# Performance work log

Hardware: AMD Instinct MI355X
Metric: run time of the kernel (lower is better)

Reference implementation:

```python
import jax, jax.numpy as jnp
import numpy as np

B, C, H, W = 16, 192, 48, 48
D_STATE, DT_RANK, D_INNER, K = 16, 16, 288, 4


def setup_inputs() -> dict:
    key = jax.random.key(0)
    ks = jax.random.split(key, 8)
    g = lambda k, shape, scale: jax.random.normal(k, shape, jnp.float32) * scale
    # S4D-real style init: A_log = log(1..N)
    A_log = jnp.tile(jnp.log(jnp.arange(1.0, D_STATE + 1.0, dtype=jnp.float32)), (K, D_INNER, 1))
    return {
        "x": jax.random.normal(ks[0], (B, C, H, W), jnp.float32),
        "W_in": g(ks[1], (C, 2 * D_INNER), C ** -0.5),
        "conv_w": g(ks[2], (D_INNER, 1, 3, 3), 1.0 / 3.0),
        "conv_b": jnp.zeros((D_INNER,), jnp.float32),
        "x_proj_w": g(ks[3], (K, DT_RANK + 2 * D_STATE, D_INNER), D_INNER ** -0.5),
        "dt_w": g(ks[4], (K, D_INNER, DT_RANK), DT_RANK ** -0.5),
        "dt_b": g(ks[5], (K, D_INNER), 0.5) - 4.0,
        "A_log": A_log,
        "Ds": jnp.ones((K, D_INNER), jnp.float32),
        "ln_g": jnp.ones((D_INNER,), jnp.float32),
        "ln_b": jnp.zeros((D_INNER,), jnp.float32),
        "W_out": g(ks[6], (D_INNER, C), D_INNER ** -0.5),
        "bn_g": jnp.ones((C,), jnp.float32),
        "bn_b": jnp.zeros((C,), jnp.float32),
    }


def reference(x, W_in, conv_w, conv_b, x_proj_w, dt_w, dt_b, A_log, Ds,
              ln_g, ln_b, W_out, bn_g, bn_b):
    b, c, h, w = x.shape
    L = h * w
    # MambaBlock: NCHW -> NHWC, SS2D(v2), NHWC -> NCHW, BatchNorm2d
    xhwc = jnp.transpose(x, (0, 2, 3, 1))                        # (B,H,W,C)
    xz = xhwc @ W_in                                             # (B,H,W,2*Di)
    xc, z = jnp.split(xz, 2, axis=-1)
    # depthwise 3x3 conv + SiLU
    xc = jnp.transpose(xc, (0, 3, 1, 2))                         # (B,Di,H,W)
    xc = jax.lax.conv_general_dilated(
        xc, conv_w, (1, 1), ((1, 1), (1, 1)),
        dimension_numbers=('NCHW', 'OIHW', 'NCHW'),
        feature_group_count=D_INNER)
    xc = jax.nn.silu(xc + conv_b[None, :, None, None])
    # cross-scan: 4 directions (row-major, col-major, + reversals)
    x_hw = xc.reshape(b, D_INNER, L)
    x_wh = jnp.transpose(xc, (0, 1, 3, 2)).reshape(b, D_INNER, L)
    xs = jnp.stack([x_hw, x_wh], axis=1)
    xs = jnp.concatenate([xs, jnp.flip(xs, axis=-1)], axis=1)    # (B,K,Di,L)
    # input-dependent dt, B, C
    x_dbl = jnp.einsum('bkdl,kcd->bkcl', xs, x_proj_w)
    dts, Bmat, Cmat = jnp.split(x_dbl, [DT_RANK, DT_RANK + D_STATE], axis=2)
    dt = jnp.einsum('bkrl,kdr->bkdl', dts, dt_w)
    dt = jax.nn.softplus(dt + dt_b[None, :, :, None])            # (B,K,Di,L)
    A = -jnp.exp(A_log)                                          # (K,Di,N)
    # selective scan along L (sequential recurrence)
    us = jnp.transpose(xs, (3, 0, 1, 2))                         # (L,B,K,Di)
    dts_t = jnp.transpose(dt, (3, 0, 1, 2))
    Bs_t = jnp.transpose(Bmat, (3, 0, 1, 2))                     # (L,B,K,N)
    Cs_t = jnp.transpose(Cmat, (3, 0, 1, 2))

    def step(hst, inp):
        u_t, d_t, B_t, C_t = inp
        dA = jnp.exp(d_t[..., None] * A)                         # (B,K,Di,N)
        hst = dA * hst + (d_t * u_t)[..., None] * B_t[:, :, None, :]
        y_t = jnp.sum(hst * C_t[:, :, None, :], axis=-1)         # (B,K,Di)
        return hst, y_t

    h0 = jnp.zeros((b, K, D_INNER, D_STATE), xs.dtype)
    _, ys = jax.lax.scan(step, h0, (us, dts_t, Bs_t, Cs_t))
    ys = jnp.transpose(ys, (1, 2, 3, 0))                         # (B,K,Di,L)
    ys = ys + Ds[None, :, :, None] * xs                          # skip (D) term
    # cross-merge: undo flips / transpose and sum the 4 directions
    y = ys[:, 0] + jnp.flip(ys[:, 2], axis=-1)
    y_wh = ys[:, 1] + jnp.flip(ys[:, 3], axis=-1)                # col-major order
    y = y + jnp.transpose(y_wh.reshape(b, D_INNER, w, h), (0, 1, 3, 2)).reshape(b, D_INNER, L)
    y = jnp.transpose(y.reshape(b, D_INNER, h, w), (0, 2, 3, 1))  # (B,H,W,Di)
    # out_norm (LayerNorm over channels), gating, out projection
    mu = jnp.mean(y, axis=-1, keepdims=True)
    var = jnp.var(y, axis=-1, keepdims=True)
    y = (y - mu) * jax.lax.rsqrt(var + 1e-5) * ln_g + ln_b
    y = y * jax.nn.silu(z)
    out = jnp.transpose(y @ W_out, (0, 3, 1, 2))                 # (B,C,H,W)
    # BatchNorm2d (training-mode batch statistics)
    m = jnp.mean(out, axis=(0, 2, 3), keepdims=True)
    v = jnp.var(out, axis=(0, 2, 3), keepdims=True)
    out = (out - m) * jax.lax.rsqrt(v + 1e-5) * bn_g[None, :, None, None] + bn_b[None, :, None, None]
    return out
```

## Files before the change

### kernel.cpp

```cpp
#include <hip/hip_runtime.h>
#include <hip/hip_fp16.h>
#include <math.h>

#define BB 16
#define CC 192
#define LL 2304
#define DI 288
#define NS 16

__device__ __forceinline__ float softplus_f(float v) {
  return v > 15.f ? v : __logf(1.f + __expf(v));
}

__device__ __forceinline__ int pos_of(int k, int t) {
  int tt = (k >= 2) ? (2303 - t) : t;
  if (k & 1) return (tt % 48) * 48 + tt / 48;
  return tt;
}
__device__ __forceinline__ int invpos(int k, int l) {
  int tt = (k & 1) ? (l % 48) * 48 + l / 48 : l;
  return (k >= 2) ? (2303 - tt) : tt;
}

__device__ __forceinline__ void pow_table(float E, float* P) {
  float p2 = E * E, p4 = p2 * p2, p8 = p4 * p4;
  P[0] = E;       P[1] = p2;      P[2] = p2 * E;  P[3] = p4;
  P[4] = p4 * E;  P[5] = p4 * p2; P[6] = p4 * P[2]; P[7] = p8;
  P[8] = p8 * E;  P[9] = p8 * p2; P[10] = p8 * P[2]; P[11] = p8 * p4;
  P[12] = p8 * P[4]; P[13] = p8 * P[5]; P[14] = p8 * P[6]; P[15] = p8 * p8;
}

__global__ __launch_bounds__(256) void k_wT(const float* __restrict__ xpw,
                                            float* __restrict__ wT) {
  int i = blockIdx.x * 256 + threadIdx.x;
  if (i >= DI * CC) return;
  int d = i % DI, j = i / DI;
  wT[d * CC + j] = xpw[j * DI + d];
}

__global__ __launch_bounds__(256) void k_check(const float* __restrict__ alog,
                                               int* __restrict__ flag) {
  __shared__ int ok;
  if (threadIdx.x == 0) ok = 1;
  __syncthreads();
  int bad = 0;
  for (int i = threadIdx.x; i < 4 * DI * NS; i += 256) {
    int n = i & 15;
    float t = __logf((float)(n + 1));
    if (fabsf(alog[i] - t) > 1e-5f) bad = 1;
  }
  if (bad) atomicAnd(&ok, 0);
  __syncthreads();
  if (threadIdx.x == 0) *flag = ok;
}

__global__ __launch_bounds__(256) void g_inproj(const float* __restrict__ x,
                                                const float* __restrict__ Win,
                                                float* __restrict__ xc,
                                                float* __restrict__ z) {
  __shared__ float Asm[48 * 128];
  __shared__ float Bsm[48 * 64];
  int nt = blockIdx.x % 9, mt = blockIdx.x / 9;
  int b = mt / 18, l0 = (mt % 18) * 128;
  int j0 = nt * 64;
  int tl = threadIdx.x & 15, tj = threadIdx.x >> 4;
  float acc[8][4];
#pragma unroll
  for (int i = 0; i < 8; ++i)
#pragma unroll
    for (int m = 0; m < 4; ++m) acc[i][m] = 0.f;
  for (int kt = 0; kt < 4; ++kt) {
    int k0 = kt * 48;
    __syncthreads();
    for (int i = threadIdx.x; i < 1536; i += 256) {
      int c = i >> 5, lq = i & 31;
      *(float4*)&Asm[c * 128 + lq * 4] =
          *(const float4*)&x[((size_t)b * CC + k0 + c) * LL + l0 + lq * 4];
    }
    for (int i = threadIdx.x; i < 768; i += 256) {
      int c = i >> 4, jq = i & 15;
      *(float4*)&Bsm[c * 64 + jq * 4] =
          *(const float4*)&Win[(size_t)(k0 + c) * 576 + j0 + jq * 4];
    }
    __syncthreads();
    for (int k = 0; k < 48; ++k) {
      float4 a0 = *(float4*)&Asm[k * 128 + tl * 8];
      float4 a1 = *(float4*)&Asm[k * 128 + tl * 8 + 4];
      float4 bv = *(float4*)&Bsm[k * 64 + tj * 4];
      float av[8] = {a0.x, a0.y, a0.z, a0.w, a1.x, a1.y, a1.z, a1.w};
      float bw[4] = {bv.x, bv.y, bv.z, bv.w};
#pragma unroll
      for (int i = 0; i < 8; ++i)
#pragma unroll
        for (int m = 0; m < 4; ++m) acc[i][m] = fmaf(av[i], bw[m], acc[i][m]);
    }
  }
  int jbase = j0 + tj * 4;
  if (jbase < DI) {
#pragma unroll
    for (int i = 0; i < 8; ++i) {
      int l = l0 + tl * 8 + i;
      *(float4*)&xc[((size_t)b * LL + l) * DI + jbase] =
          make_float4(acc[i][0], acc[i][1], acc[i][2], acc[i][3]);
    }
  } else {
    int j2 = jbase - DI;
#pragma unroll
    for (int m = 0; m < 4; ++m) {
      *(float4*)&z[((size_t)b * DI + j2 + m) * LL + l0 + tl * 8] =
          make_float4(acc[0][m], acc[1][m], acc[2][m], acc[3][m]);
      *(float4*)&z[((size_t)b * DI + j2 + m) * LL + l0 + tl * 8 + 4] =
          make_float4(acc[4][m], acc[5][m], acc[6][m], acc[7][m]);
    }
  }
}

__global__ __launch_bounds__(288) void k_conv2(const float* __restrict__ xc,
                                               const float* __restrict__ cw,
                                               const float* __restrict__ cb,
                                               float* __restrict__ co) {
  int b = blockIdx.x / 48, h = blockIdx.x % 48;
  int d = threadIdx.x;
  float wv[9];
#pragma unroll
  for (int j = 0; j < 9; ++j) wv[j] = cw[d * 9 + j];
  float bias = cb[d];
  bool hm = h > 0, hp = h < 47;
  const float* row0 = xc + ((size_t)b * LL + (h - 1) * 48) * DI + d;
  const float* row1 = xc + ((size_t)b * LL + h * 48) * DI + d;
  const float* row2 = xc + ((size_t)b * LL + (h + 1) * 48) * DI + d;
  float* op = co + ((size_t)b * LL + h * 48) * DI + d;
  float a0 = 0.f, a1 = 0.f, a2 = 0.f;
  float b0, b1, b2, c0, c1, c2;
  b0 = hm ? row0[0] : 0.f;
  b1 = row1[0];
  b2 = hp ? row2[0] : 0.f;
  for (int w = 0; w < 48; ++w) {
    if (w < 47) {
      int off = (w + 1) * DI;
      c0 = hm ? row0[off] : 0.f;
      c1 = row1[off];
      c2 = hp ? row2[off] : 0.f;
    } else {
      c0 = 0.f; c1 = 0.f; c2 = 0.f;
    }
    float acc = bias;
    acc = fmaf(a0, wv[0], acc); acc = fmaf(b0, wv[1], acc); acc = fmaf(c0, wv[2], acc);
    acc = fmaf(a1, wv[3], acc); acc = fmaf(b1, wv[4], acc); acc = fmaf(c1, wv[5], acc);
    acc = fmaf(a2, wv[6], acc); acc = fmaf(b2, wv[7], acc); acc = fmaf(c2, wv[8], acc);
    acc = acc / (1.f + __expf(-acc));
    op[w * DI] = acc;
    a0 = b0; a1 = b1; a2 = b2;
    b0 = c0; b1 = c1; b2 = c2;
  }
}

__global__ __launch_bounds__(256) void g_xdbl(const float* __restrict__ co,
                                              const float* __restrict__ wT,
                                              float* __restrict__ xd) {
  __shared__ float Asm[48 * 132];
  __shared__ float Bsm[48 * 64];
  int nt = blockIdx.x % 3, mt = blockIdx.x / 3;
  int b = mt / 18, l0 = (mt % 18) * 128;
  int j0 = nt * 64;
  int tl = threadIdx.x & 15, tj = threadIdx.x >> 4;
  float acc[8][4];
#pragma unroll
  for (int i = 0; i < 8; ++i)
#pragma unroll
    for (int m = 0; m < 4; ++m) acc[i][m] = 0.f;
  for (int kt = 0; kt < 6; ++kt) {
    int k0 = kt * 48;
    __syncthreads();
    for (int i = threadIdx.x; i < 1536; i += 256) {
      int l = i / 12, dq = i % 12;
      float4 v = *(const float4*)&co[((size_t)b * LL + l0 + l) * DI + k0 + dq * 4];
      Asm[(dq * 4 + 0) * 132 + l] = v.x;
      Asm[(dq * 4 + 1) * 132 + l] = v.y;
      Asm[(dq * 4 + 2) * 132 + l] = v.z;
      Asm[(dq * 4 + 3) * 132 + l] = v.w;
    }
    for (int i = threadIdx.x; i < 768; i += 256) {
      int c = i >> 4, jq = i & 15;
      *(float4*)&Bsm[c * 64 + jq * 4] =
          *(const float4*)&wT[(size_t)(k0 + c) * CC + j0 + jq * 4];
    }
    __syncthreads();
    for (int k = 0; k < 48; ++k) {
      float4 a0 = *(float4*)&Asm[k * 132 + tl * 8];
      float4 a1 = *(float4*)&Asm[k * 132 + tl * 8 + 4];
      float4 bv = *(float4*)&Bsm[k * 64 + tj * 4];
      float av[8] = {a0.x, a0.y, a0.z, a0.w, a1.x, a1.y, a1.z, a1.w};
      float bw[4] = {bv.x, bv.y, bv.z, bv.w};
#pragma unroll
      for (int i = 0; i < 8; ++i)
#pragma unroll
        for (int m = 0; m < 4; ++m) acc[i][m] = fmaf(av[i], bw[m], acc[i][m]);
    }
  }
  int j = j0 + tj * 4;
  int kk = j / 48, c2 = j % 48;
#pragma unroll
  for (int i = 0; i < 8; ++i) {
    int l = l0 + tl * 8 + i;
    *(float4*)&xd[(((size_t)b * 4 + kk) * LL + l) * 48 + c2] =
        make_float4(acc[i][0], acc[i][1], acc[i][2], acc[i][3]);
  }
}

__global__ __launch_bounds__(288) void g_dt(const float* __restrict__ xd,
                                            const float* __restrict__ dtw,
                                            const float* __restrict__ dtb,
                                            __half* __restrict__ dth) {
  int blk = blockIdx.x;
  int lc = blk % 72, bk = blk / 72;
  int k = bk & 3;
  int d = threadIdx.x;
  float w_dt[16];
#pragma unroll
  for (int r4 = 0; r4 < 4; ++r4) {
    float4 t4 = *(const float4*)&dtw[((size_t)k * DI + d) * 16 + r4 * 4];
    w_dt[r4 * 4 + 0] = t4.x; w_dt[r4 * 4 + 1] = t4.y;
    w_dt[r4 * 4 + 2] = t4.z; w_dt[r4 * 4 + 3] = t4.w;
  }
  float bias = dtb[k * DI + d];
  const float* __restrict__ xb = xd + (size_t)bk * LL * 48;
  __half* __restrict__ Eb = dth + (size_t)bk * LL * DI;
#pragma unroll 2
  for (int j = 0; j < 32; ++j) {
    int l = lc * 32 + j;
    const float* __restrict__ xr = xb + (size_t)l * 48;
    float4 v0 = *(const float4*)(xr + 0);
    float4 v1 = *(const float4*)(xr + 4);
    float4 v2 = *(const float4*)(xr + 8);
    float4 v3 = *(const float4*)(xr + 12);
    float a0 = fmaf(v0.x, w_dt[0], bias);
    float a1 = v0.y * w_dt[1];
    float a2 = v0.z * w_dt[2];
    float a3 = v0.w * w_dt[3];
    a0 = fmaf(v1.x, w_dt[4], a0); a1 = fmaf(v1.y, w_dt[5], a1);
    a2 = fmaf(v1.z, w_dt[6], a2); a3 = fmaf(v1.w, w_dt[7], a3);
    a0 = fmaf(v2.x, w_dt[8], a0); a1 = fmaf(v2.y, w_dt[9], a1);
    a2 = fmaf(v2.z, w_dt[10], a2); a3 = fmaf(v2.w, w_dt[11], a3);
    a0 = fmaf(v3.x, w_dt[12], a0); a1 = fmaf(v3.y, w_dt[13], a1);
    a2 = fmaf(v3.z, w_dt[14], a2); a3 = fmaf(v3.w, w_dt[15], a3);
    float v = (a0 + a1) + (a2 + a3);
    float dt = v > 15.f ? v : __logf(1.f + __expf(v));
    int t = invpos(k, l);
    Eb[(size_t)t * DI + d] = __float2half(dt);
  }
}

template <int SCHT, bool USE_E>
__global__ __launch_bounds__(288) void k_pass1(const float* __restrict__ co,
                                               const float* __restrict__ xd,
                                               const float* __restrict__ dtw,
                                               const float* __restrict__ dtb,
                                               const float* __restrict__ alog,
                                               const int* __restrict__ flag,
                                               const __half* __restrict__ dth,
                                               float* __restrict__ HL,
                                               float* __restrict__ Sd) {
  constexpr int TCHT = LL / SCHT;
  int blk = blockIdx.x;
  int s = blk % SCHT, k = (blk / SCHT) & 3, b = blk / (SCHT * 4);
  int d = threadIdx.x;
  float w_dt[16];
  float bias = 0.f;
  if constexpr (!USE_E) {
#pragma unroll
    for (int r4 = 0; r4 < 4; ++r4) {
      float4 t4 = *(const float4*)&dtw[((size_t)k * DI + d) * 16 + r4 * 4];
      w_dt[r4 * 4 + 0] = t4.x; w_dt[r4 * 4 + 1] = t4.y;
      w_dt[r4 * 4 + 2] = t4.z; w_dt[r4 * 4 + 3] = t4.w;
    }
    bias = dtb[k * DI + d];
  }
  float h[16];
#pragma unroll
  for (int n = 0; n < 16; ++n) h[n] = 0.f;
  const float* __restrict__ xb = xd + ((size_t)b * 4 + k) * LL * 48;
  const float* __restrict__ cb_ = co + (size_t)b * LL * DI;
  const __half* __restrict__ Eb = dth + ((size_t)b * 4 + k) * LL * DI;
  int fast = *flag;
  size_t base = ((size_t)((b * 4 + k) * SCHT + s) * DI + d) * 16;
  size_t sbase = ((size_t)((b * 4 + k) * SCHT + s) * DI + d);
  float S = 0.f;
  if (fast) {
    for (int i = 0; i < TCHT; ++i) {
      int t = s * TCHT + i;
      int l = __builtin_amdgcn_readfirstlane(pos_of(k, t));
      const float* __restrict__ xr = xb + (size_t)l * 48;
      float4 q0 = *(const float4*)(xr + 16);
      float4 q1 = *(const float4*)(xr + 20);
      float4 q2 = *(const float4*)(xr + 24);
      float4 q3 = *(const float4*)(xr + 28);
      float u = cb_[(size_t)l * DI + d];
      float E, dt;
      if constexpr (USE_E) {
        dt = __half2float(Eb[(size_t)t * DI + d]);
        E = __expf(-dt);
      } else {
        float4 v0 = *(const float4*)(xr + 0);
        float4 v1 = *(const float4*)(xr + 4);
        float4 v2 = *(const float4*)(xr + 8);
        float4 v3 = *(const float4*)(xr + 12);
        float a0 = fmaf(v0.x, w_dt[0], bias), a1 = v0.y * w_dt[1];
        float a2 = v0.z * w_dt[2], a3 = v0.w * w_dt[3];
        a0 = fmaf(v1.x, w_dt[4], a0); a1 = fmaf(v1.y, w_dt[5], a1);
        a2 = fmaf(v1.z, w_dt[6], a2); a3 = fmaf(v1.w, w_dt[7], a3);
        a0 = fmaf(v2.x, w_dt[8], a0); a1 = fmaf(v2.y, w_dt[9], a1);
        a2 = fmaf(v2.z, w_dt[10], a2); a3 = fmaf(v2.w, w_dt[11], a3);
        a0 = fmaf(v3.x, w_dt[12], a0); a1 = fmaf(v3.y, w_dt[13], a1);
        a2 = fmaf(v3.z, w_dt[14], a2); a3 = fmaf(v3.w, w_dt[15], a3);
        float v = (a0 + a1) + (a2 + a3);
        float ev = __expf(v);
        E = __builtin_amdgcn_rcpf(1.f + ev);
        dt = v > 15.f ? v : __logf(1.f + ev);
      }
      float xv = dt * u;
      S += dt;
      float P[16];
      pow_table(E, P);
      float Bv[16] = {q0.x, q0.y, q0.z, q0.w, q1.x, q1.y, q1.z, q1.w,
                      q2.x, q2.y, q2.z, q2.w, q3.x, q3.y, q3.z, q3.w};
#pragma unroll
      for (int n = 0; n < 16; ++n) h[n] = fmaf(P[n], h[n], xv * Bv[n]);
    }
  } else {
    float A[16];
#pragma unroll
    for (int n = 0; n < 16; ++n) A[n] = -__expf(alog[((size_t)k * DI + d) * 16 + n]);
    for (int i = 0; i < TCHT; ++i) {
      int t = s * TCHT + i;
      int l = __builtin_amdgcn_readfirstlane(pos_of(k, t));
      const float* __restrict__ xr = xb + (size_t)l * 48;
      float4 q0 = *(const float4*)(xr + 16);
      float4 q1 = *(const float4*)(xr + 20);
      float4 q2 = *(const float4*)(xr + 24);
      float4 q3 = *(const float4*)(xr + 28);
      float u = cb_[(size_t)l * DI + d];
      float dt;
      if constexpr (USE_E) {
        dt = __half2float(Eb[(size_t)t * DI + d]);
      } else {
        float a0 = bias, a1 = 0.f, a2 = 0.f, a3 = 0.f;
#pragma unroll
        for (int r = 0; r < 4; ++r) {
          a0 = fmaf(xr[r * 4 + 0], w_dt[r * 4 + 0], a0);
          a1 = fmaf(xr[r * 4 + 1], w_dt[r * 4 + 1], a1);
          a2 = fmaf(xr[r * 4 + 2], w_dt[r * 4 + 2], a2);
          a3 = fmaf(xr[r * 4 + 3], w_dt[r * 4 + 3], a3);
        }
        dt = softplus_f((a0 + a1) + (a2 + a3));
      }
      float xv = dt * u;
      S += dt;
      float Bv[16] = {q0.x, q0.y, q0.z, q0.w, q1.x, q1.y, q1.z, q1.w,
                      q2.x, q2.y, q2.z, q2.w, q3.x, q3.y, q3.z, q3.w};
#pragma unroll
      for (int n = 0; n < 16; ++n) {
        float dA = __expf(dt * A[n]);
        h[n] = fmaf(dA, h[n], xv * Bv[n]);
      }
    }
  }
  Sd[sbase] = S;
#pragma unroll
  for (int n = 0; n < 16; ++n) HL[base + n] = h[n];
}

template <int SCHT>
__global__ __launch_bounds__(256) void k_stitch(float* __restrict__ HL,
                                                const float* __restrict__ Sd,
                                                const float* __restrict__ alog,
                                                const int* __restrict__ flag) {
  int idx = blockIdx.x * 256 + threadIdx.x;
  if (idx >= 64 * DI) return;
  int d = idx % DI, bk = idx / DI;
  int k = bk & 3;
  int fast = *flag;
  float A[16];
  if (!fast) {
#pragma unroll
    for (int n = 0; n < 16; ++n) A[n] = -__expf(alog[((size_t)k * DI + d) * 16 + n]);
  }
  float h[16];
#pragma unroll
  for (int n = 0; n < 16; ++n) h[n] = 0.f;
  for (int s = 0; s < SCHT; ++s) {
    size_t base = ((size_t)(bk * SCHT + s) * DI + d) * 16;
    float S = Sd[(size_t)(bk * SCHT + s) * DI + d];
    float Q[16];
    if (fast) {
      pow_table(__expf(-S), Q);
    } else {
#pragma unroll
      for (int n = 0; n < 16; ++n) Q[n] = __expf(A[n] * S);
    }
#pragma unroll
    for (int n = 0; n < 16; ++n) {
      float hl = HL[base + n];
      HL[base + n] = h[n];
      h[n] = fmaf(Q[n], h[n], hl);
    }
  }
}

template <int SCHT, bool USE_E>
__global__ __launch_bounds__(288) void k_pass2(const float* __restrict__ co,
                                               const float* __restrict__ xd,
                                               const float* __restrict__ dtw,
                                               const float* __restrict__ dtb,
                                               const float* __restrict__ alog,
                                               const int* __restrict__ flag,
                                               const __half* __restrict__ dth,
                                               const float* __restrict__ Hin,
                                               float* __restrict__ ym) {
  constexpr int TCHT = LL / SCHT;
  int blk = blockIdx.x;
  int s = blk % SCHT, k = (blk / SCHT) & 3, b = blk / (SCHT * 4);
  int d = threadIdx.x;
  float w_dt[16];
  float bias = 0.f;
  if constexpr (!USE_E) {
#pragma unroll
    for (int r4 = 0; r4 < 4; ++r4) {
      float4 t4 = *(const float4*)&dtw[((size_t)k * DI + d) * 16 + r4 * 4];
      w_dt[r4 * 4 + 0] = t4.x; w_dt[r4 * 4 + 1] = t4.y;
      w_dt[r4 * 4 + 2] = t4.z; w_dt[r4 * 4 + 3] = t4.w;
    }
    bias = dtb[k * DI + d];
  }
  size_t base = ((size_t)((b * 4 + k) * SCHT + s) * DI + d) * 16;
  float h[16];
#pragma unroll
  for (int n = 0; n < 16; ++n) h[n] = Hin[base + n];
  const float* __restrict__ xb = xd + ((size_t)b * 4 + k) * LL * 48;
  const float* __restrict__ cb_ = co + (size_t)b * LL * DI;
  const __half* __restrict__ Eb = dth + ((size_t)b * 4 + k) * LL * DI;
  float* __restrict__ yb = ym + (size_t)b * LL * DI;
  int fast = *flag;
  if (fast) {
    for (int i = 0; i < TCHT; ++i) {
      int t = s * TCHT + i;
      int l = __builtin_amdgcn_readfirstlane(pos_of(k, t));
      const float* __restrict__ xr = xb + (size_t)l * 48;
      float4 q0 = *(const float4*)(xr + 16);
      float4 q1 = *(const float4*)(xr + 20);
      float4 q2 = *(const float4*)(xr + 24);
      float4 q3 = *(const float4*)(xr + 28);
      float4 c0 = *(const float4*)(xr + 32);
      float4 c1 = *(const float4*)(xr + 36);
      float4 c2 = *(const float4*)(xr + 40);
      float4 c3 = *(const float4*)(xr + 44);
      float u = cb_[(size_t)l * DI + d];
      float E, dt;
      if constexpr (USE_E) {
        dt = __half2float(Eb[(size_t)t * DI + d]);
        E = __expf(-dt);
      } else {
        float4 v0 = *(const float4*)(xr + 0);
        float4 v1 = *(const float4*)(xr + 4);
        float4 v2 = *(const float4*)(xr + 8);
        float4 v3 = *(const float4*)(xr + 12);
        float a0 = fmaf(v0.x, w_dt[0], bias), a1 = v0.y * w_dt[1];
        float a2 = v0.z * w_dt[2], a3 = v0.w * w_dt[3];
        a0 = fmaf(v1.x, w_dt[4], a0); a1 = fmaf(v1.y, w_dt[5], a1);
        a2 = fmaf(v1.z, w_dt[6], a2); a3 = fmaf(v1.w, w_dt[7], a3);
        a0 = fmaf(v2.x, w_dt[8], a0); a1 = fmaf(v2.y, w_dt[9], a1);
        a2 = fmaf(v2.z, w_dt[10], a2); a3 = fmaf(v2.w, w_dt[11], a3);
        a0 = fmaf(v3.x, w_dt[12], a0); a1 = fmaf(v3.y, w_dt[13], a1);
        a2 = fmaf(v3.z, w_dt[14], a2); a3 = fmaf(v3.w, w_dt[15], a3);
        float v = (a0 + a1) + (a2 + a3);
        float ev = __expf(v);
        E = __builtin_amdgcn_rcpf(1.f + ev);
        dt = v > 15.f ? v : __logf(1.f + ev);
      }
      float xv = dt * u;
      float P[16];
      pow_table(E, P);
      float Bv[16] = {q0.x, q0.y, q0.z, q0.w, q1.x, q1.y, q1.z, q1.w,
                      q2.x, q2.y, q2.z, q2.w, q3.x, q3.y, q3.z, q3.w};
      float Cv[16] = {c0.x, c0.y, c0.z, c0.w, c1.x, c1.y, c1.z, c1.w,
                      c2.x, c2.y, c2.z, c2.w, c3.x, c3.y, c3.z, c3.w};
      float y0 = 0.f, y1 = 0.f, y2 = 0.f, y3 = 0.f;
#pragma unroll
      for (int n = 0; n < 16; n += 4) {
        h[n + 0] = fmaf(P[n + 0], h[n + 0], xv * Bv[n + 0]);
        h[n + 1] = fmaf(P[n + 1], h[n + 1], xv * Bv[n + 1]);
        h[n + 2] = fmaf(P[n + 2], h[n + 2], xv * Bv[n + 2]);
        h[n + 3] = fmaf(P[n + 3], h[n + 3], xv * Bv[n + 3]);
        y0 = fmaf(h[n + 0], Cv[n + 0], y0);
        y1 = fmaf(h[n + 1], Cv[n + 1], y1);
        y2 = fmaf(h[n + 2], Cv[n + 2], y2);
        y3 = fmaf(h[n + 3], Cv[n + 3], y3);
      }
      atomicAdd(&yb[(size_t)l * DI + d], (y0 + y1) + (y2 + y3));
    }
  } else {
    float A[16];
#pragma unroll
    for (int n = 0; n < 16; ++n) A[n] = -__expf(alog[((size_t)k * DI + d) * 16 + n]);
    for (int i = 0; i < TCHT; ++i) {
      int t = s * TCHT + i;
      int l = __builtin_amdgcn_readfirstlane(pos_of(k, t));
      const float* __restrict__ xr = xb + (size_t)l * 48;
      float4 q0 = *(const float4*)(xr + 16);
      float4 q1 = *(const float4*)(xr + 20);
      float4 q2 = *(const float4*)(xr + 24);
      float4 q3 = *(const float4*)(xr + 28);
      float4 c0 = *(const float4*)(xr + 32);
      float4 c1 = *(const float4*)(xr + 36);
      float4 c2 = *(const float4*)(xr + 40);
      float4 c3 = *(const float4*)(xr + 44);
      float u = cb_[(size_t)l * DI + d];
      float dt;
      if constexpr (USE_E) {
        dt = __half2float(Eb[(size_t)t * DI + d]);
      } else {
        float a0 = bias, a1 = 0.f, a2 = 0.f, a3 = 0.f;
#pragma unroll
        for (int r = 0; r < 4; ++r) {
          a0 = fmaf(xr[r * 4 + 0], w_dt[r * 4 + 0], a0);
          a1 = fmaf(xr[r * 4 + 1], w_dt[r * 4 + 1], a1);
          a2 = fmaf(xr[r * 4 + 2], w_dt[r * 4 + 2], a2);
          a3 = fmaf(xr[r * 4 + 3], w_dt[r * 4 + 3], a3);
        }
        dt = softplus_f((a0 + a1) + (a2 + a3));
      }
      float xv = dt * u;
      float Bv[16] = {q0.x, q0.y, q0.z, q0.w, q1.x, q1.y, q1.z, q1.w,
                      q2.x, q2.y, q2.z, q2.w, q3.x, q3.y, q3.z, q3.w};
      float Cv[16] = {c0.x, c0.y, c0.z, c0.w, c1.x, c1.y, c1.z, c1.w,
                      c2.x, c2.y, c2.z, c2.w, c3.x, c3.y, c3.z, c3.w};
      float y = 0.f;
#pragma unroll
      for (int n = 0; n < 16; ++n) {
        float dA = __expf(dt * A[n]);
        h[n] = fmaf(dA, h[n], xv * Bv[n]);
        y = fmaf(h[n], Cv[n], y);
      }
      atomicAdd(&yb[(size_t)l * DI + d], y);
    }
  }
}

__global__ __launch_bounds__(256) void k_ln(const float* __restrict__ ym,
                                            const float* __restrict__ co,
                                            const float* __restrict__ z,
                                            const float* __restrict__ Ds,
                                            const float* __restrict__ lng,
                                            const float* __restrict__ lnb,
                                            float* __restrict__ Yt) {
  __shared__ float As[DI * 33];
  __shared__ float red[512];
  __shared__ float mus[32], rss[32];
  int b = blockIdx.x / 72;
  int l0 = (blockIdx.x % 72) * 32;
  for (int i = threadIdx.x; i < DI * 32; i += 256) {
    int l = i / DI, d = i % DI;
    float sds = Ds[d] + Ds[DI + d] + Ds[2 * DI + d] + Ds[3 * DI + d];
    size_t off = ((size_t)b * LL + l0 + l) * DI + d;
    As[d * 33 + l] = ym[off] + sds * co[off];
  }
  __syncthreads();
  int l = threadIdx.x & 31;
  int p = threadIdx.x >> 5;
  float s1 = 0.f, s2 = 0.f;
  for (int d = p; d < DI; d += 8) {
    float v = As[d * 33 + l];
    s1 += v; s2 += v * v;
  }
  red[p * 32 + l] = s1;
  red[256 + p * 32 + l] = s2;
  __syncthreads();
  if (threadIdx.x < 32) {
    float su = 0.f, sq = 0.f;
#pragma unroll
    for (int q = 0; q < 8; ++q) { su += red[q * 32 + l]; sq += red[256 + q * 32 + l]; }
    float mu = su * (1.f / 288.f);
    float var = sq * (1.f / 288.f) - mu * mu;
    mus[l] = mu;
    rss[l] = rsqrtf(var + 1e-5f);
  }
  __syncthreads();
  {
    float mu = mus[l], rs = rss[l];
    for (int d = p; d < DI; d += 8) {
      float v = (As[d * 33 + l] - mu) * rs * lng[d] + lnb[d];
      float zv = z[((size_t)b * DI + d) * LL + l0 + l];
      v *= zv / (1.f + __expf(-zv));
      As[d * 33 + l] = v;
    }
  }
  __syncthreads();
  for (int i = threadIdx.x; i < DI * 32; i += 256) {
    int d = i >> 5, ll = i & 31;
    Yt[((size_t)b * DI + d) * LL + l0 + ll] = As[d * 33 + ll];
  }
}

__global__ __launch_bounds__(256) void g_outproj(const float* __restrict__ Yt,
                                                 const float* __restrict__ Wout,
                                                 float* __restrict__ out,
                                                 float* __restrict__ bnsum,
                                                 float* __restrict__ bnsq) {
  __shared__ float Asm[48 * 128];
  __shared__ float Bsm[48 * 64];
  int nt = blockIdx.x % 3, mt = blockIdx.x / 3;
  int b = mt / 18, l0 = (mt % 18) * 128;
  int j0 = nt * 64;
  int tl = threadIdx.x & 15, tj = threadIdx.x >> 4;
  float acc[8][4];
#pragma unroll
  for (int i = 0; i < 8; ++i)
#pragma unroll
    for (int m = 0; m < 4; ++m) acc[i][m] = 0.f;
  for (int kt = 0; kt < 6; ++kt) {
    int k0 = kt * 48;
    __syncthreads();
    for (int i = threadIdx.x; i < 1536; i += 256) {
      int c = i >> 5, lq = i & 31;
      *(float4*)&Asm[c * 128 + lq * 4] =
          *(const float4*)&Yt[((size_t)b * DI + k0 + c) * LL + l0 + lq * 4];
    }
    for (int i = threadIdx.x; i < 768; i += 256) {
      int c = i >> 4, jq = i & 15;
      *(float4*)&Bsm[c * 64 + jq * 4] =
          *(const float4*)&Wout[(size_t)(k0 + c) * CC + j0 + jq * 4];
    }
    __syncthreads();
    for (int k = 0; k < 48; ++k) {
      float4 a0 = *(float4*)&Asm[k * 128 + tl * 8];
      float4 a1 = *(float4*)&Asm[k * 128 + tl * 8 + 4];
      float4 bv = *(float4*)&Bsm[k * 64 + tj * 4];
      float av[8] = {a0.x, a0.y, a0.z, a0.w, a1.x, a1.y, a1.z, a1.w};
      float bw[4] = {bv.x, bv.y, bv.z, bv.w};
#pragma unroll
      for (int i = 0; i < 8; ++i)
#pragma unroll
        for (int m = 0; m < 4; ++m) acc[i][m] = fmaf(av[i], bw[m], acc[i][m]);
    }
  }
#pragma unroll
  for (int m = 0; m < 4; ++m) {
    int j = j0 + tj * 4 + m;
    *(float4*)&out[((size_t)b * CC + j) * LL + l0 + tl * 8] =
        make_float4(acc[0][m], acc[1][m], acc[2][m], acc[3][m]);
    *(float4*)&out[((size_t)b * CC + j) * LL + l0 + tl * 8 + 4] =
        make_float4(acc[4][m], acc[5][m], acc[6][m], acc[7][m]);
    float r1 = 0.f, r2 = 0.f;
#pragma unroll
    for (int i = 0; i < 8; ++i) { r1 += acc[i][m]; r2 += acc[i][m] * acc[i][m]; }
#pragma unroll
    for (int o = 1; o < 16; o <<= 1) {
      r1 += __shfl_xor(r1, o);
      r2 += __shfl_xor(r2, o);
    }
    if (tl == 0) {
      atomicAdd(&bnsum[j], r1);
      atomicAdd(&bnsq[j], r2);
    }
  }
}

__global__ __launch_bounds__(256) void k_bnfin(float* __restrict__ out,
                                               const float* __restrict__ bnsum,
                                               const float* __restrict__ bnsq,
                                               const float* __restrict__ bg,
                                               const float* __restrict__ bb) {
  int idx = blockIdx.x * 256 + threadIdx.x;
  int c = (idx / LL) % CC;
  float mean = bnsum[c] * (1.f / 36864.f);
  float var = bnsq[c] * (1.f / 36864.f) - mean * mean;
  float sc = bg[c] * rsqrtf(var + 1e-5f);
  out[idx] = (out[idx] - mean) * sc + bb[c];
}

extern "C" void kernel_launch(void* const* d_in, const int* in_sizes, int n_in,
                              void* d_out, int out_size, void* d_ws, size_t ws_size,
                              hipStream_t stream) {
  (void)in_sizes; (void)n_in; (void)out_size;
  const float* x    = (const float*)d_in[0];
  const float* Win  = (const float*)d_in[1];
  const float* cw   = (const float*)d_in[2];
  const float* cbb  = (const float*)d_in[3];
  const float* xpw  = (const float*)d_in[4];
  const float* dtw  = (const float*)d_in[5];
  const float* dtb  = (const float*)d_in[6];
  const float* alog = (const float*)d_in[7];
  const float* Ds   = (const float*)d_in[8];
  const float* lng  = (const float*)d_in[9];
  const float* lnb  = (const float*)d_in[10];
  const float* Wout = (const float*)d_in[11];
  const float* bg   = (const float*)d_in[12];
  const float* bb   = (const float*)d_in[13];
  float* out = (float*)d_out;

  const size_t NXC = 10616832, NXD = 7077888, NWT = 55296;
  const size_t NE  = 42467328;
  const size_t REH = NE / 2;
  auto hlN = [](int sch) { return (size_t)64 * sch * DI * 16; };
  auto sdN = [](int sch) { return (size_t)64 * sch * DI; };
  auto needE = [&](int sch) {
    return (3 * NXC + NXD + REH + NWT + hlN(sch) + sdN(sch) + 1024) * 4;
  };
  auto needN = [&](int sch) {
    return (3 * NXC + NXD + NWT + hlN(sch) + sdN(sch) + 1024) * 4;
  };
  bool useE; int sch;
  if (ws_size >= needE(32))      { useE = true;  sch = 32; }
  else if (ws_size >= needE(16)) { useE = true;  sch = 16; }
  else if (ws_size >= needN(32)) { useE = false; sch = 32; }
  else                           { useE = false; sch = 16; }

  float* ws = (float*)d_ws;
  float* z  = ws;
  float* A1 = z + NXC;
  float* co = A1 + NXC;
  float* xd = co + NXC;
  float* R  = xd + NXD;
  float *xc, *ym, *wT;
  __half* dth = nullptr;
  if (useE) {
    xc = R;
    ym = A1;
    dth = (__half*)R;
    wT = R + REH;
  } else {
    xc = A1; ym = A1;
    wT = R;
  }
  float* HL = wT + NWT;
  float* Sd = HL + hlN(sch);
  float* bnsum = Sd + sdN(sch);
  float* bnsq  = bnsum + 192;
  int*   flag  = (int*)(bnsq + 192);
  float* Yt = xd;

  k_wT<<<216, 256, 0, stream>>>(xpw, wT);
  k_check<<<1, 256, 0, stream>>>(alog, flag);
  g_inproj<<<2592, 256, 0, stream>>>(x, Win, xc, z);
  k_conv2<<<768, 288, 0, stream>>>(xc, cw, cbb, co);
  hipMemsetAsync(ym, 0, NXC * 4, stream);
  hipMemsetAsync(bnsum, 0, 2 * 192 * 4, stream);
  g_xdbl<<<864, 256, 0, stream>>>(co, wT, xd);
  if (useE) g_dt<<<4608, 288, 0, stream>>>(xd, dtw, dtb, dth);
  if (useE && sch == 32) {
    k_pass1<32, true><<<2048, 288, 0, stream>>>(co, xd, dtw, dtb, alog, flag, dth, HL, Sd);
    k_stitch<32><<<72, 256, 0, stream>>>(HL, Sd, alog, flag);
    k_pass2<32, true><<<2048, 288, 0, stream>>>(co, xd, dtw, dtb, alog, flag, dth, HL, ym);
  } else if (useE) {
    k_pass1<16, true><<<1024, 288, 0, stream>>>(co, xd, dtw, dtb, alog, flag, dth, HL, Sd);
    k_stitch<16><<<72, 256, 0, stream>>>(HL, Sd, alog, flag);
    k_pass2<16, true><<<1024, 288, 0, stream>>>(co, xd, dtw, dtb, alog, flag, dth, HL, ym);
  } else if (sch == 32) {
    k_pass1<32, false><<<2048, 288, 0, stream>>>(co, xd, dtw, dtb, alog, flag, dth, HL, Sd);
    k_stitch<32><<<72, 256, 0, stream>>>(HL, Sd, alog, flag);
    k_pass2<32, false><<<2048, 288, 0, stream>>>(co, xd, dtw, dtb, alog, flag, dth, HL, ym);
  } else {
    k_pass1<16, false><<<1024, 288, 0, stream>>>(co, xd, dtw, dtb, alog, flag, dth, HL, Sd);
    k_stitch<16><<<72, 256, 0, stream>>>(HL, Sd, alog, flag);
    k_pass2<16, false><<<1024, 288, 0, stream>>>(co, xd, dtw, dtb, alog, flag, dth, HL, ym);
  }
  k_ln<<<1152, 256, 0, stream>>>(ym, co, z, Ds, lng, lnb, Yt);
  g_outproj<<<864, 256, 0, stream>>>(Yt, Wout, out, bnsum, bnsq);
  k_bnfin<<<27648, 256, 0, stream>>>(out, bnsum, bnsq, bg, bb);
}
```

Before: 785.8 us.

## Convert the three dense projections to bf16 MFMA with pre-converted weights

The in-projection, x_proj and out-projection GEMMs move from fp32 FMA tiling to bf16 MFMA 16x16x32 instructions. A prep kernel converts and transposes the weights to bf16 once per call, and activations are converted to bf16 as they are staged into LDS. k_ln now writes its output in (B,L,Di) layout so the out-projection's A tile can be read along K. Outputs go through LDS so the NCHW tensors can be stored with vector writes and the BatchNorm partial sums can be taken from LDS. The aim is to cut GEMM compute time, at the cost of bf16 rounding error in the projections, which then feed a sensitive scan.

```diff
diff --git a/kernel.cpp b/kernel.cpp
--- a/kernel.cpp
+++ b/kernel.cpp
@@ -7,6 +7,15 @@
 #define LL 2304
 #define DI 288
 #define NS 16
+
+typedef float f32x4 __attribute__((ext_vector_type(4)));
+typedef short bf16x8 __attribute__((ext_vector_type(8)));
+
+__device__ __forceinline__ short f2b(float f) {
+  union { float f; unsigned u; } x; x.f = f;
+  unsigned r = x.u + 0x7FFF + ((x.u >> 16) & 1);
+  return (short)(r >> 16);
+}
 
 __device__ __forceinline__ float softplus_f(float v) {
   return v > 15.f ? v : __logf(1.f + __expf(v));
@@ -30,12 +39,24 @@
   P[12] = p8 * P[4]; P[13] = p8 * P[5]; P[14] = p8 * P[6]; P[15] = p8 * p8;
 }
 
-__global__ __launch_bounds__(256) void k_wT(const float* __restrict__ xpw,
-                                            float* __restrict__ wT) {
+__global__ __launch_bounds__(256) void k_wprep(const float* __restrict__ Win,
+                                               const float* __restrict__ xpw,
+                                               const float* __restrict__ Wout,
+                                               short* __restrict__ winb,
+                                               short* __restrict__ xpwb,
+                                               short* __restrict__ woutb) {
   int i = blockIdx.x * 256 + threadIdx.x;
-  if (i >= DI * CC) return;
-  int d = i % DI, j = i / DI;
-  wT[d * CC + j] = xpw[j * DI + d];
+  if (i < 110592) {
+    int j = i / 192, c = i % 192;
+    winb[i] = f2b(Win[(size_t)c * 576 + j]);
+  } else if (i < 165888) {
+    int t = i - 110592;
+    xpwb[t] = f2b(xpw[t]);
+  } else {
+    int t = i - 165888;
+    int j = t / 288, d = t % 288;
+    woutb[t] = f2b(Wout[(size_t)d * 192 + j]);
+  }
 }
 
 __global__ __launch_bounds__(256) void k_check(const float* __restrict__ alog,
@@ -55,62 +76,69 @@
 }
 
 __global__ __launch_bounds__(256) void g_inproj(const float* __restrict__ x,
-                                                const float* __restrict__ Win,
+                                                const short* __restrict__ winb,
                                                 float* __restrict__ xc,
                                                 float* __restrict__ z) {
-  __shared__ float Asm[48 * 128];
-  __shared__ float Bsm[48 * 64];
-  int nt = blockIdx.x % 9, mt = blockIdx.x / 9;
-  int b = mt / 18, l0 = (mt % 18) * 128;
-  int j0 = nt * 64;
-  int tl = threadIdx.x & 15, tj = threadIdx.x >> 4;
-  float acc[8][4];
-#pragma unroll
-  for (int i = 0; i < 8; ++i)
-#pragma unroll
-    for (int m = 0; m < 4; ++m) acc[i][m] = 0.f;
-  for (int kt = 0; kt < 4; ++kt) {
-    int k0 = kt * 48;
+  __shared__ short As[64 * 200];
+  __shared__ short Bs[48 * 200];
+  int nt = blockIdx.x % 12, mt = blockIdx.x / 12;
+  int b = mt / 36, l0 = (mt % 36) * 64;
+  int j0 = nt * 48;
+  int tid = threadIdx.x;
+  for (int i = tid; i < 3072; i += 256) {
+    int c = i >> 4, lq = i & 15;
+    float4 v = *(const float4*)&x[((size_t)b * CC + c) * LL + l0 + lq * 4];
+    As[(lq * 4 + 0) * 200 + c] = f2b(v.x);
+    As[(lq * 4 + 1) * 200 + c] = f2b(v.y);
+    As[(lq * 4 + 2) * 200 + c] = f2b(v.z);
+    As[(lq * 4 + 3) * 200 + c] = f2b(v.w);
+  }
+  for (int i = tid; i < 1152; i += 256) {
+    int n = i / 24, kq = i % 24;
+    *(bf16x8*)&Bs[n * 200 + kq * 8] =
+        *(const bf16x8*)&winb[(size_t)(j0 + n) * 192 + kq * 8];
+  }
+  __syncthreads();
+  int w = tid >> 6, lane = tid & 63;
+  int ln = lane & 15, q8 = (lane >> 4) * 8;
+  int m0 = w * 16;
+  f32x4 acc0 = {0.f, 0.f, 0.f, 0.f}, acc1 = acc0, acc2 = acc0;
+#pragma unroll
+  for (int kt = 0; kt < 6; ++kt) {
+    bf16x8 a = *(bf16x8*)&As[(m0 + ln) * 200 + kt * 32 + q8];
+    bf16x8 b0 = *(bf16x8*)&Bs[(0 * 16 + ln) * 200 + kt * 32 + q8];
+    bf16x8 b1 = *(bf16x8*)&Bs[(1 * 16 + ln) * 200 + kt * 32 + q8];
+    bf16x8 b2 = *(bf16x8*)&Bs[(2 * 16 + ln) * 200 + kt * 32 + q8];
+    acc0 = __builtin_amdgcn_mfma_f32_16x16x32_bf16(a, b0, acc0, 0, 0, 0);
+    acc1 = __builtin_amdgcn_mfma_f32_16x16x32_bf16(a, b1, acc1, 0, 0, 0);
+    acc2 = __builtin_amdgcn_mfma_f32_16x16x32_bf16(a, b2, acc2, 0, 0, 0);
+  }
+  int mrow = m0 + (lane >> 4) * 4;
+  if (nt < 6) {
+#pragma unroll
+    for (int r = 0; r < 4; ++r) {
+      size_t rb = ((size_t)b * LL + l0 + mrow + r) * DI + j0;
+      xc[rb + 0 * 16 + ln] = acc0[r];
+      xc[rb + 1 * 16 + ln] = acc1[r];
+      xc[rb + 2 * 16 + ln] = acc2[r];
+    }
+  } else {
     __syncthreads();
-    for (int i = threadIdx.x; i < 1536; i += 256) {
-      int c = i >> 5, lq = i & 31;
-      *(float4*)&Asm[c * 128 + lq * 4] =
-          *(const float4*)&x[((size_t)b * CC + k0 + c) * LL + l0 + lq * 4];
-    }
-    for (int i = threadIdx.x; i < 768; i += 256) {
-      int c = i >> 4, jq = i & 15;
-      *(float4*)&Bsm[c * 64 + jq * 4] =
-          *(const float4*)&Win[(size_t)(k0 + c) * 576 + j0 + jq * 4];
+    float* Zs = (float*)As;
+#pragma unroll
+    for (int r = 0; r < 4; ++r) {
+      int lm = mrow + r - 0;
+      Zs[(0 * 16 + ln) * 66 + lm] = acc0[r];
+      Zs[(1 * 16 + ln) * 66 + lm] = acc1[r];
+      Zs[(2 * 16 + ln) * 66 + lm] = acc2[r];
     }
     __syncthreads();
-    for (int k = 0; k < 48; ++k) {
-      float4 a0 = *(float4*)&Asm[k * 128 + tl * 8];
-      float4 a1 = *(float4*)&Asm[k * 128 + tl * 8 + 4];
-      float4 bv = *(float4*)&Bsm[k * 64 + tj * 4];
-      float av[8] = {a0.x, a0.y, a0.z, a0.w, a1.x, a1.y, a1.z, a1.w};
-      float bw[4] = {bv.x, bv.y, bv.z, bv.w};
-#pragma unroll
-      for (int i = 0; i < 8; ++i)
-#pragma unroll
-        for (int m = 0; m < 4; ++m) acc[i][m] = fmaf(av[i], bw[m], acc[i][m]);
-    }
-  }
-  int jbase = j0 + tj * 4;
-  if (jbase < DI) {
-#pragma unroll
-    for (int i = 0; i < 8; ++i) {
-      int l = l0 + tl * 8 + i;
-      *(float4*)&xc[((size_t)b * LL + l) * DI + jbase] =
-          make_float4(acc[i][0], acc[i][1], acc[i][2], acc[i][3]);
-    }
-  } else {
-    int j2 = jbase - DI;
-#pragma unroll
-    for (int m = 0; m < 4; ++m) {
-      *(float4*)&z[((size_t)b * DI + j2 + m) * LL + l0 + tl * 8] =
-          make_float4(acc[0][m], acc[1][m], acc[2][m], acc[3][m]);
-      *(float4*)&z[((size_t)b * DI + j2 + m) * LL + l0 + tl * 8 + 4] =
-          make_float4(acc[4][m], acc[5][m], acc[6][m], acc[7][m]);
+    int j2base = j0 - DI;
+    for (int i = tid; i < 768; i += 256) {
+      int j = i >> 4, lq = i & 15;
+      float4 v = make_float4(Zs[j * 66 + lq * 4 + 0], Zs[j * 66 + lq * 4 + 1],
+                             Zs[j * 66 + lq * 4 + 2], Zs[j * 66 + lq * 4 + 3]);
+      *(float4*)&z[((size_t)b * DI + j2base + j) * LL + l0 + lq * 4] = v;
     }
   }
 }
@@ -156,55 +184,51 @@
 }
 
 __global__ __launch_bounds__(256) void g_xdbl(const float* __restrict__ co,
-                                              const float* __restrict__ wT,
+                                              const short* __restrict__ xpwb,
                                               float* __restrict__ xd) {
-  __shared__ float Asm[48 * 132];
-  __shared__ float Bsm[48 * 64];
-  int nt = blockIdx.x % 3, mt = blockIdx.x / 3;
-  int b = mt / 18, l0 = (mt % 18) * 128;
-  int j0 = nt * 64;
-  int tl = threadIdx.x & 15, tj = threadIdx.x >> 4;
-  float acc[8][4];
-#pragma unroll
-  for (int i = 0; i < 8; ++i)
-#pragma unroll
-    for (int m = 0; m < 4; ++m) acc[i][m] = 0.f;
-  for (int kt = 0; kt < 6; ++kt) {
-    int k0 = kt * 48;
-    __syncthreads();
-    for (int i = threadIdx.x; i < 1536; i += 256) {
-      int l = i / 12, dq = i % 12;
-      float4 v = *(const float4*)&co[((size_t)b * LL + l0 + l) * DI + k0 + dq * 4];
-      Asm[(dq * 4 + 0) * 132 + l] = v.x;
-      Asm[(dq * 4 + 1) * 132 + l] = v.y;
-      Asm[(dq * 4 + 2) * 132 + l] = v.z;
-      Asm[(dq * 4 + 3) * 132 + l] = v.w;
-    }
-    for (int i = threadIdx.x; i < 768; i += 256) {
-      int c = i >> 4, jq = i & 15;
-      *(float4*)&Bsm[c * 64 + jq * 4] =
-          *(const float4*)&wT[(size_t)(k0 + c) * CC + j0 + jq * 4];
-    }
-    __syncthreads();
-    for (int k = 0; k < 48; ++k) {
-      float4 a0 = *(float4*)&Asm[k * 132 + tl * 8];
-      float4 a1 = *(float4*)&Asm[k * 132 + tl * 8 + 4];
-      float4 bv = *(float4*)&Bsm[k * 64 + tj * 4];
-      float av[8] = {a0.x, a0.y, a0.z, a0.w, a1.x, a1.y, a1.z, a1.w};
-      float bw[4] = {bv.x, bv.y, bv.z, bv.w};
-#pragma unroll
-      for (int i = 0; i < 8; ++i)
-#pragma unroll
-        for (int m = 0; m < 4; ++m) acc[i][m] = fmaf(av[i], bw[m], acc[i][m]);
-    }
-  }
-  int j = j0 + tj * 4;
-  int kk = j / 48, c2 = j % 48;
-#pragma unroll
-  for (int i = 0; i < 8; ++i) {
-    int l = l0 + tl * 8 + i;
-    *(float4*)&xd[(((size_t)b * 4 + kk) * LL + l) * 48 + c2] =
-        make_float4(acc[i][0], acc[i][1], acc[i][2], acc[i][3]);
+  __shared__ short As[64 * 296];
+  __shared__ short Bs[48 * 296];
+  int nt = blockIdx.x % 4, mt = blockIdx.x / 4;
+  int b = mt / 36, l0 = (mt % 36) * 64;
+  int j0 = nt * 48;
+  int tid = threadIdx.x;
+  for (int i = tid; i < 2304; i += 256) {
+    int m = i / 36, kq = i % 36;
+    const float* src = &co[((size_t)b * LL + l0 + m) * DI + kq * 8];
+    float4 f0 = *(const float4*)src;
+    float4 f1 = *(const float4*)(src + 4);
+    bf16x8 v;
+    v[0] = f2b(f0.x); v[1] = f2b(f0.y); v[2] = f2b(f0.z); v[3] = f2b(f0.w);
+    v[4] = f2b(f1.x); v[5] = f2b(f1.y); v[6] = f2b(f1.z); v[7] = f2b(f1.w);
+    *(bf16x8*)&As[m * 296 + kq * 8] = v;
+  }
+  for (int i = tid; i < 1728; i += 256) {
+    int n = i / 36, kq = i % 36;
+    *(bf16x8*)&Bs[n * 296 + kq * 8] =
+        *(const bf16x8*)&xpwb[(size_t)(j0 + n) * 288 + kq * 8];
+  }
+  __syncthreads();
+  int w = tid >> 6, lane = tid & 63;
+  int ln = lane & 15, q8 = (lane >> 4) * 8;
+  int m0 = w * 16;
+  f32x4 acc0 = {0.f, 0.f, 0.f, 0.f}, acc1 = acc0, acc2 = acc0;
+#pragma unroll
+  for (int kt = 0; kt < 9; ++kt) {
+    bf16x8 a = *(bf16x8*)&As[(m0 + ln) * 296 + kt * 32 + q8];
+    bf16x8 b0 = *(bf16x8*)&Bs[(0 * 16 + ln) * 296 + kt * 32 + q8];
+    bf16x8 b1 = *(bf16x8*)&Bs[(1 * 16 + ln) * 296 + kt * 32 + q8];
+    bf16x8 b2 = *(bf16x8*)&Bs[(2 * 16 + ln) * 296 + kt * 32 + q8];
+    acc0 = __builtin_amdgcn_mfma_f32_16x16x32_bf16(a, b0, acc0, 0, 0, 0);
+    acc1 = __builtin_amdgcn_mfma_f32_16x16x32_bf16(a, b1, acc1, 0, 0, 0);
+    acc2 = __builtin_amdgcn_mfma_f32_16x16x32_bf16(a, b2, acc2, 0, 0, 0);
+  }
+  int mrow = m0 + (lane >> 4) * 4;
+#pragma unroll
+  for (int r = 0; r < 4; ++r) {
+    size_t rb = (((size_t)b * 4 + nt) * LL + l0 + mrow + r) * 48;
+    xd[rb + 0 * 16 + ln] = acc0[r];
+    xd[rb + 1 * 16 + ln] = acc1[r];
+    xd[rb + 2 * 16 + ln] = acc2[r];
   }
 }
 
@@ -552,7 +576,7 @@
                                             const float* __restrict__ Ds,
                                             const float* __restrict__ lng,
                                             const float* __restrict__ lnb,
-                                            float* __restrict__ Yt) {
+                                            float* __restrict__ Yl) {
   __shared__ float As[DI * 33];
   __shared__ float red[512];
   __shared__ float mus[32], rss[32];
@@ -596,72 +620,77 @@
   }
   __syncthreads();
   for (int i = threadIdx.x; i < DI * 32; i += 256) {
-    int d = i >> 5, ll = i & 31;
-    Yt[((size_t)b * DI + d) * LL + l0 + ll] = As[d * 33 + ll];
-  }
-}
-
-__global__ __launch_bounds__(256) void g_outproj(const float* __restrict__ Yt,
-                                                 const float* __restrict__ Wout,
+    int ll = i / DI, d = i % DI;
+    Yl[((size_t)b * LL + l0 + ll) * DI + d] = As[d * 33 + ll];
+  }
+}
+
+__global__ __launch_bounds__(256) void g_outproj(const float* __restrict__ Yl,
+                                                 const short* __restrict__ woutb,
                                                  float* __restrict__ out,
                                                  float* __restrict__ bnsum,
                                                  float* __restrict__ bnsq) {
-  __shared__ float Asm[48 * 128];
-  __shared__ float Bsm[48 * 64];
-  int nt = blockIdx.x % 3, mt = blockIdx.x / 3;
-  int b = mt / 18, l0 = (mt % 18) * 128;
-  int j0 = nt * 64;
-  int tl = threadIdx.x & 15, tj = threadIdx.x >> 4;
-  float acc[8][4];
-#pragma unroll
-  for (int i = 0; i < 8; ++i)
-#pragma unroll
-    for (int m = 0; m < 4; ++m) acc[i][m] = 0.f;
-  for (int kt = 0; kt < 6; ++kt) {
-    int k0 = kt * 48;
-    __syncthreads();
-    for (int i = threadIdx.x; i < 1536; i += 256) {
-      int c = i >> 5, lq = i & 31;
-      *(float4*)&Asm[c * 128 + lq * 4] =
-          *(const float4*)&Yt[((size_t)b * DI + k0 + c) * LL + l0 + lq * 4];
-    }
-    for (int i = threadIdx.x; i < 768; i += 256) {
-      int c = i >> 4, jq = i & 15;
-      *(float4*)&Bsm[c * 64 + jq * 4] =
-          *(const float4*)&Wout[(size_t)(k0 + c) * CC + j0 + jq * 4];
-    }
-    __syncthreads();
-    for (int k = 0; k < 48; ++k) {
-      float4 a0 = *(float4*)&Asm[k * 128 + tl * 8];
-      float4 a1 = *(float4*)&Asm[k * 128 + tl * 8 + 4];
-      float4 bv = *(float4*)&Bsm[k * 64 + tj * 4];
-      float av[8] = {a0.x, a0.y, a0.z, a0.w, a1.x, a1.y, a1.z, a1.w};
-      float bw[4] = {bv.x, bv.y, bv.z, bv.w};
-#pragma unroll
-      for (int i = 0; i < 8; ++i)
-#pragma unroll
-        for (int m = 0; m < 4; ++m) acc[i][m] = fmaf(av[i], bw[m], acc[i][m]);
-    }
-  }
-#pragma unroll
-  for (int m = 0; m < 4; ++m) {
-    int j = j0 + tj * 4 + m;
-    *(float4*)&out[((size_t)b * CC + j) * LL + l0 + tl * 8] =
-        make_float4(acc[0][m], acc[1][m], acc[2][m], acc[3][m]);
-    *(float4*)&out[((size_t)b * CC + j) * LL + l0 + tl * 8 + 4] =
-        make_float4(acc[4][m], acc[5][m], acc[6][m], acc[7][m]);
-    float r1 = 0.f, r2 = 0.f;
-#pragma unroll
-    for (int i = 0; i < 8; ++i) { r1 += acc[i][m]; r2 += acc[i][m] * acc[i][m]; }
-#pragma unroll
-    for (int o = 1; o < 16; o <<= 1) {
-      r1 += __shfl_xor(r1, o);
-      r2 += __shfl_xor(r2, o);
-    }
-    if (tl == 0) {
-      atomicAdd(&bnsum[j], r1);
-      atomicAdd(&bnsq[j], r2);
-    }
+  __shared__ short As[64 * 296];
+  __shared__ short Bs[48 * 296];
+  int nt = blockIdx.x % 4, mt = blockIdx.x / 4;
+  int b = mt / 36, l0 = (mt % 36) * 64;
+  int j0 = nt * 48;
+  int tid = threadIdx.x;
+  for (int i = tid; i < 2304; i += 256) {
+    int m = i / 36, kq = i % 36;
+    const float* src = &Yl[((size_t)b * LL + l0 + m) * DI + kq * 8];
+    float4 f0 = *(const float4*)src;
+    float4 f1 = *(const float4*)(src + 4);
+    bf16x8 v;
+    v[0] = f2b(f0.x); v[1] = f2b(f0.y); v[2] = f2b(f0.z); v[3] = f2b(f0.w);
+    v[4] = f2b(f1.x); v[5] = f2b(f1.y); v[6] = f2b(f1.z); v[7] = f2b(f1.w);
+    *(bf16x8*)&As[m * 296 + kq * 8] = v;
+  }
+  for (int i = tid; i < 1728; i += 256) {
+    int n = i / 36, kq = i % 36;
+    *(bf16x8*)&Bs[n * 296 + kq * 8] =
+        *(const bf16x8*)&woutb[(size_t)(j0 + n) * 288 + kq * 8];
+  }
+  __syncthreads();
+  int w = tid >> 6, lane = tid & 63;
+  int ln = lane & 15, q8 = (lane >> 4) * 8;
+  int m0 = w * 16;
+  f32x4 acc0 = {0.f, 0.f, 0.f, 0.f}, acc1 = acc0, acc2 = acc0;
+#pragma unroll
+  for (int kt = 0; kt < 9; ++kt) {
+    bf16x8 a = *(bf16x8*)&As[(m0 + ln) * 296 + kt * 32 + q8];
+    bf16x8 b0 = *(bf16x8*)&Bs[(0 * 16 + ln) * 296 + kt * 32 + q8];
+    bf16x8 b1 = *(bf16x8*)&Bs[(1 * 16 + ln) * 296 + kt * 32 + q8];
+    bf16x8 b2 = *(bf16x8*)&Bs[(2 * 16 + ln) * 296 + kt * 32 + q8];
+    acc0 = __builtin_amdgcn_mfma_f32_16x16x32_bf16(a, b0, acc0, 0, 0, 0);
+    acc1 = __builtin_amdgcn_mfma_f32_16x16x32_bf16(a, b1, acc1, 0, 0, 0);
+    acc2 = __builtin_amdgcn_mfma_f32_16x16x32_bf16(a, b2, acc2, 0, 0, 0);
+  }
+  __syncthreads();
+  float* Zs = (float*)As;
+  int lm = m0 + (lane >> 4) * 4;
+#pragma unroll
+  for (int r = 0; r < 4; ++r) {
+    Zs[(0 * 16 + ln) * 66 + lm + r] = acc0[r];
+    Zs[(1 * 16 + ln) * 66 + lm + r] = acc1[r];
+    Zs[(2 * 16 + ln) * 66 + lm + r] = acc2[r];
+  }
+  __syncthreads();
+  for (int i = tid; i < 768; i += 256) {
+    int j = i >> 4, lq = i & 15;
+    float4 v = make_float4(Zs[j * 66 + lq * 4 + 0], Zs[j * 66 + lq * 4 + 1],
+                           Zs[j * 66 + lq * 4 + 2], Zs[j * 66 + lq * 4 + 3]);
+    *(float4*)&out[((size_t)b * CC + j0 + j) * LL + l0 + lq * 4] = v;
+  }
+  if (tid < 48) {
+    float s1 = 0.f, s2 = 0.f;
+#pragma unroll 8
+    for (int l = 0; l < 64; ++l) {
+      float v = Zs[tid * 66 + l];
+      s1 += v; s2 += v * v;
+    }
+    atomicAdd(&bnsum[j0 + tid], s1);
+    atomicAdd(&bnsq[j0 + tid], s2);
   }
 }
 
@@ -698,16 +727,17 @@
   const float* bb   = (const float*)d_in[13];
   float* out = (float*)d_out;
 
-  const size_t NXC = 10616832, NXD = 7077888, NWT = 55296;
+  const size_t NXC = 10616832, NXD = 7077888;
+  const size_t NWB = 110592;
   const size_t NE  = 42467328;
   const size_t REH = NE / 2;
   auto hlN = [](int sch) { return (size_t)64 * sch * DI * 16; };
   auto sdN = [](int sch) { return (size_t)64 * sch * DI; };
   auto needE = [&](int sch) {
-    return (3 * NXC + NXD + REH + NWT + hlN(sch) + sdN(sch) + 1024) * 4;
+    return (3 * NXC + NWB + NXD + REH + hlN(sch) + sdN(sch) + 1024) * 4;
   };
   auto needN = [&](int sch) {
-    return (3 * NXC + NXD + NWT + hlN(sch) + sdN(sch) + 1024) * 4;
+    return (3 * NXC + NWB + NXD + hlN(sch) + sdN(sch) + 1024) * 4;
   };
   bool useE; int sch;
   if (ws_size >= needE(32))      { useE = true;  sch = 32; }
@@ -716,36 +746,40 @@
   else                           { useE = false; sch = 16; }
 
   float* ws = (float*)d_ws;
-  float* z  = ws;
-  float* A1 = z + NXC;
-  float* co = A1 + NXC;
-  float* xd = co + NXC;
-  float* R  = xd + NXD;
-  float *xc, *ym, *wT;
+  float* z   = ws;
+  float* A1  = z + NXC;
+  float* co  = A1 + NXC;
+  float* wbF = co + NXC;
+  float* xd  = wbF + NWB;
+  float* R   = xd + NXD;
+  short* winb  = (short*)wbF;
+  short* xpwb  = (short*)(wbF + 55296);
+  short* woutb = (short*)(wbF + 55296 + 27648);
+  float *xc, *ym, *tail;
   __half* dth = nullptr;
   if (useE) {
     xc = R;
     ym = A1;
     dth = (__half*)R;
-    wT = R + REH;
+    tail = R + REH;
   } else {
     xc = A1; ym = A1;
-    wT = R;
-  }
-  float* HL = wT + NWT;
+    tail = R;
+  }
+  float* HL = tail;
   float* Sd = HL + hlN(sch);
   float* bnsum = Sd + sdN(sch);
   float* bnsq  = bnsum + 192;
   int*   flag  = (int*)(bnsq + 192);
-  float* Yt = xd;
-
-  k_wT<<<216, 256, 0, stream>>>(xpw, wT);
+  float* Yl = xd;
+
+  k_wprep<<<864, 256, 0, stream>>>(Win, xpw, Wout, winb, xpwb, woutb);
   k_check<<<1, 256, 0, stream>>>(alog, flag);
-  g_inproj<<<2592, 256, 0, stream>>>(x, Win, xc, z);
+  g_inproj<<<6912, 256, 0, stream>>>(x, winb, xc, z);
   k_conv2<<<768, 288, 0, stream>>>(xc, cw, cbb, co);
   hipMemsetAsync(ym, 0, NXC * 4, stream);
   hipMemsetAsync(bnsum, 0, 2 * 192 * 4, stream);
-  g_xdbl<<<864, 256, 0, stream>>>(co, wT, xd);
+  g_xdbl<<<2304, 256, 0, stream>>>(co, xpwb, xd);
   if (useE) g_dt<<<4608, 288, 0, stream>>>(xd, dtw, dtb, dth);
   if (useE && sch == 32) {
     k_pass1<32, true><<<2048, 288, 0, stream>>>(co, xd, dtw, dtb, alog, flag, dth, HL, Sd);
@@ -764,7 +798,7 @@
     k_stitch<16><<<72, 256, 0, stream>>>(HL, Sd, alog, flag);
     k_pass2<16, false><<<1024, 288, 0, stream>>>(co, xd, dtw, dtb, alog, flag, dth, HL, ym);
   }
-  k_ln<<<1152, 256, 0, stream>>>(ym, co, z, Ds, lng, lnb, Yt);
-  g_outproj<<<864, 256, 0, stream>>>(Yt, Wout, out, bnsum, bnsq);
+  k_ln<<<1152, 256, 0, stream>>>(ym, co, z, Ds, lng, lnb, Yl);
+  g_outproj<<<2304, 256, 0, stream>>>(Yl, woutb, out, bnsum, bnsq);
   k_bnfin<<<27648, 256, 0, stream>>>(out, bnsum, bnsq, bg, bb);
 }
```

Measured after the change: 708.6 us. 9.8% less time.
